# Kernel optimization log

Measured on AMD Instinct MI355X. Metric: run time of the kernel, lower is better.

## Reference

```python
import math
import jax, jax.numpy as jnp
import numpy as np

N_HEAD = 4
D_MODEL = 96
BS, N_TOK = 32, 512
A2LEN = 150          # a2len % 16 != 0 so padn > 0 (asserted in torch code)
DST_MXLEN = 32


def setup_inputs() -> dict:
    key = jax.random.key(0)
    k1, k2, k3, k4, k5, k6 = jax.random.split(key, 6)
    x = jax.random.normal(k1, (BS, N_TOK, D_MODEL), dtype=jnp.float32)
    # LinearM: w is [outdim, indim+1], last column is the bias, zeroed at init
    wqv_w = 0.02 * jax.random.normal(k2, (3 * D_MODEL, D_MODEL + 1), dtype=jnp.float32)
    wqv_w = wqv_w.at[:, -1].set(0.0)
    fanout_w = 0.02 * jax.random.normal(k3, (D_MODEL, D_MODEL + 1), dtype=jnp.float32)
    fanout_w = fanout_w.at[:, -1].set(0.0)

    def make_coo(k):
        # COO triples [dst, src, dst_cnt]; every dst has DST_MXLEN sources
        dst = jnp.repeat(jnp.arange(N_TOK), DST_MXLEN)
        src = jax.random.randint(k, (N_TOK * DST_MXLEN,), 0, N_TOK)
        cnt = jnp.tile(jnp.arange(DST_MXLEN), N_TOK)
        return jnp.stack([dst, src, cnt], axis=1).astype(jnp.int32)

    coo0 = make_coo(k4)
    coo1 = make_coo(k5)
    a2a = jnp.sort(jax.random.permutation(k6, N_TOK)[:A2LEN]).astype(jnp.int32)
    return {"x": x, "wqv_w": wqv_w, "fanout_w": fanout_w,
            "coo0": coo0, "coo1": coo1, "a2a": a2a, "dst_mxlen": DST_MXLEN}


def _linm(w, x):
    # LinearM: einsum('oi,bhi->bho') + bias column
    return jnp.einsum('oi,bti->bto', w[:, :-1], x) + w[:, -1]


def _l1attn_sparse(v, q, k, coo, dst_mxlen):
    # l1attn_sparse_cuda.L1AttnSparse: per-(dst,src) L1 scores scattered into a
    # [n_tok, dst_mxlen] ragged table (pad = -1e12), softmax over the fan-in slot.
    bs, n_tok, h, w = q.shape
    dst, src, cnt = coo[:, 0], coo[:, 1], coo[:, 2]
    scale = 1.0 / math.sqrt(w)
    ww = -jnp.sum(jnp.abs(q[:, dst] - k[:, src]), axis=-1) * scale    # [bs, cl, h]
    attn = jnp.full((bs, n_tok, dst_mxlen, h), -1e12, dtype=q.dtype)
    attn = attn.at[:, dst, cnt, :].set(ww)
    attn_sm = jax.nn.softmax(attn, axis=2)
    vw = jnp.zeros((bs, n_tok, dst_mxlen, h, w), dtype=q.dtype)
    vw = vw.at[:, dst, cnt, :, :].set(v[:, src])                      # gather by src
    return jnp.einsum('bdrh,bdrhw->bdhw', attn_sm, vw)


def _forward(x, wqv_w, fanout_w, coo0, coo1, a2a, dst_mxlen):
    bs, n_tok, width = x.shape
    h = N_HEAD
    y = _linm(wqv_w, x)
    q, k, v = jnp.split(y, 3, axis=-1)

    # --- dense all-to-all L1 attention on tokens a2a, channels 72:96 (h*6) ---
    a2len = a2a.shape[0]
    q1 = q[:, a2a, 72:].reshape(bs, a2len, h, 6)
    k1 = k[:, a2a, 72:].reshape(bs, a2len, h, 6)
    v1 = v[:, a2a, 72:].reshape(bs, a2len, h, 6)
    padl = (a2len + 15) // 16 * 16
    q2 = jnp.pad(q1, ((0, 0), (0, padl - a2len), (0, 0), (0, 0)))
    k2 = jnp.pad(k1, ((0, 0), (0, padl - a2len), (0, 0), (0, 0)))
    scale = 1.0 / math.sqrt(6)
    # l1attn_cuda.L1Attn: a[b, s, d, h] = -scale * sum_w |q[b,d,h,w] - k[b,s,h,w]|
    a = -jnp.sum(jnp.abs(q2[:, None, :, :, :] - k2[:, :, None, :, :]), axis=-1) * scale
    a = a[:, :a2len + 1, :a2len + 1, :]   # keep one zero-score pad row (attention sink)
    a = jax.nn.softmax(a, axis=1)         # softmax over src dim
    a = a[:, :a2len, :a2len, :]
    b1 = jnp.einsum('bsdh,bshw->bdhw', a, v1)
    b2 = jnp.zeros((bs, n_tok, h, 6), dtype=x.dtype).at[:, a2a].set(b1)
    dense = b2.reshape(bs, n_tok, h * 6)

    # --- two sparse COO L1-attention groups: channels 32:52 and 52:72 (h*5) ---
    sparse_out = []
    for i, coo in enumerate((coo0, coo1)):
        sta = 32 + 20 * i
        q1 = q[:, :, sta:sta + 20].reshape(bs, n_tok, h, 5)
        k1 = k[:, :, sta:sta + 20].reshape(bs, n_tok, h, 5)
        v1 = v[:, :, sta:sta + 20].reshape(bs, n_tok, h, 5)
        sparse_out.append(_l1attn_sparse(v1, q1, k1, coo, dst_mxlen).reshape(bs, n_tok, h * 5))

    # channels 0:32 are never written -> zeros
    b = jnp.concatenate([jnp.zeros((bs, n_tok, 32), dtype=x.dtype),
                         sparse_out[0], sparse_out[1], dense], axis=-1)
    yb = b * jax.nn.sigmoid(1.702 * b)    # QuickGELU
    return x + _linm(fanout_w, yb)


def reference(x, wqv_w, fanout_w, coo0, coo1, a2a, dst_mxlen):
    return _forward(x, wqv_w, fanout_w, coo0, coo1, a2a, dst_mxlen)
```

## Files before the change

kernel.cpp:

```cpp
#include <hip/hip_runtime.h>
#include <hip/hip_bf16.h>
#include <math.h>

#define BS    32
#define T     512
#define BT    (BS * T)
#define D     96
#define H     4
#define MX    32
#define A2MAX 160

#define QKV_TOK  16
#define FUSE_TOK 16
#define DT       32

__global__ void prep_kernel(const float* __restrict__ wqv, const float* __restrict__ fw,
                            const int* __restrict__ coo0, const int* __restrict__ coo1,
                            const int* __restrict__ a2a, int nedges, int a2len,
                            float* __restrict__ WT, float* __restrict__ FWT,
                            int* __restrict__ srcs, int* __restrict__ flag) {
    int idx = blockIdx.x * blockDim.x + threadIdx.x;
    if (idx < 97 * 192) {
        const int i = idx / 192, oc = idx - 192 * i;
        const int p = oc >> 6, c = oc & 63;
        WT[idx] = wqv[(p * 96 + 32 + c) * 97 + i];
        return;
    }
    idx -= 97 * 192;
    if (idx < 65 * 96) {
        const int i = idx / 96, o = idx - 96 * i;
        FWT[idx] = fw[o * 97 + 32 + i];
        return;
    }
    idx -= 65 * 96;
    if (idx < 2 * nedges) {
        const int ci = idx / nedges;
        const int e  = idx - ci * nedges;
        const int* row = (ci == 0 ? coo0 : coo1) + e * 3;
        const int dst = row[0], src = row[1], cnt = row[2];
        if (dst >= 0 && dst < T && cnt >= 0 && cnt < MX)
            srcs[(ci * T + dst) * MX + cnt] = src;
        return;
    }
    idx -= 2 * nedges;
    if (idx < a2len) flag[a2a[idx]] = idx;
}

__global__ void qkv_kernel(const float* __restrict__ x, const float* __restrict__ WT,
                           const int* __restrict__ flag,
                           float* __restrict__ Q, float* __restrict__ K,
                           float* __restrict__ V,
                           float* __restrict__ Kg, float* __restrict__ Vg) {
    const int tid  = threadIdx.x;
    const int base = blockIdx.x * QKV_TOK;
    __shared__ float xs[QKV_TOK * D];
    float4* xs4 = (float4*)xs;
    const float4* xg = (const float4*)(x + base * D);
    xs4[tid]       = xg[tid];
    xs4[tid + 192] = xg[tid + 192];
    __syncthreads();
    float acc[QKV_TOK];
    const float bias = WT[96 * 192 + tid];
    #pragma unroll
    for (int j = 0; j < QKV_TOK; ++j) acc[j] = bias;
    #pragma unroll 3
    for (int i4 = 0; i4 < 24; ++i4) {
        const float w0 = WT[(4 * i4 + 0) * 192 + tid];
        const float w1 = WT[(4 * i4 + 1) * 192 + tid];
        const float w2 = WT[(4 * i4 + 2) * 192 + tid];
        const float w3 = WT[(4 * i4 + 3) * 192 + tid];
        #pragma unroll
        for (int j = 0; j < QKV_TOK; ++j) {
            const float4 xv = xs4[j * 24 + i4];
            acc[j] += w0 * xv.x + w1 * xv.y + w2 * xv.z + w3 * xv.w;
        }
    }
    const int part = tid >> 6, c = tid & 63;
    float* out = (part == 0) ? Q : (part == 1 ? K : V);
    #pragma unroll
    for (int j = 0; j < QKV_TOK; ++j) out[(base + j) * 64 + c] = acc[j];
    if (part >= 1 && c >= 40) {
        float* g = (part == 1) ? Kg : Vg;
        const int b = base >> 9;
        #pragma unroll
        for (int j = 0; j < QKV_TOK; ++j) {
            const int ps = flag[(base + j) & (T - 1)];
            if (ps >= 0) g[(b * A2MAX + ps) * 24 + (c - 40)] = acc[j];
        }
    }
}

__global__ void sparse_kernel(const float* __restrict__ Q, const float* __restrict__ K,
                              const float* __restrict__ V, const int* __restrict__ srcs,
                              float* __restrict__ B) {
    const int b   = blockIdx.y;
    const int ci  = blockIdx.x >> 2, h = blockIdx.x & 3;
    const int base = 20 * ci + h * 5;
    const int tid  = threadIdx.x;
    __shared__ float ks[5 * T];
    __shared__ float vs[5 * T];
    for (int i = tid; i < 5 * T; i += 256) {
        const int s = i & (T - 1), w = i >> 9;
        const int g = (b * T + s) * 64 + base + w;
        ks[w * T + s] = K[g];
        vs[w * T + s] = V[g];
    }
    __syncthreads();
    const float iscale = 0.4472135954999579f;
    const int t = blockIdx.z * 256 + tid;
    const int4* sp4 = (const int4*)(srcs + (ci * T + t) * MX);
    const float* qp = Q + (b * T + t) * 64 + base;
    const float q0 = qp[0], q1 = qp[1], q2 = qp[2], q3 = qp[3], q4 = qp[4];
    float l = 0.f, o0 = 0.f, o1 = 0.f, o2 = 0.f, o3 = 0.f, o4 = 0.f;
    #pragma unroll 2
    for (int c4 = 0; c4 < MX / 4; ++c4) {
        const int4 s4 = sp4[c4];
        const int sv[4] = {s4.x, s4.y, s4.z, s4.w};
        #pragma unroll
        for (int m = 0; m < 4; ++m) {
            const int s = sv[m];
            if (s < 0) continue;
            const float sum = fabsf(q0 - ks[s]) + fabsf(q1 - ks[T + s]) +
                              fabsf(q2 - ks[2 * T + s]) + fabsf(q3 - ks[3 * T + s]) +
                              fabsf(q4 - ks[4 * T + s]);
            const float e = __expf(-sum * iscale);
            l  += e;
            o0 += e * vs[s];         o1 += e * vs[T + s];
            o2 += e * vs[2 * T + s]; o3 += e * vs[3 * T + s];
            o4 += e * vs[4 * T + s];
        }
    }
    const float inv = (l > 0.f) ? 1.f / l : 0.f;
    float* bp = B + (b * T + t) * 96 + 32 + base;
    bp[0] = o0 * inv; bp[1] = o1 * inv; bp[2] = o2 * inv;
    bp[3] = o3 * inv; bp[4] = o4 * inv;
}

__global__ void dense_kernel(const float* __restrict__ Q,
                             const float* __restrict__ Kg, const float* __restrict__ Vg,
                             const int* __restrict__ a2a,
                             int a2len, int extra, float* __restrict__ B) {
    const int b   = blockIdx.y;
    const int d0  = blockIdx.x * DT;
    const int tid = threadIdx.x;
    __shared__ int   rows[A2MAX];
    __shared__ float ks[A2MAX * 32];
    __shared__ float vs[A2MAX * 32];
    for (int i = tid; i < a2len; i += 128) rows[i] = a2a[i];
    const int nq = (a2len * 24) / 4;
    const float4* kg4 = (const float4*)(Kg + (size_t)b * A2MAX * 24);
    const float4* vg4 = (const float4*)(Vg + (size_t)b * A2MAX * 24);
    for (int idx = tid; idx < nq; idx += 128) {
        const int s = idx / 6, r = idx - 6 * s;
        const float4 kk = kg4[idx];
        const float4 vv = vg4[idx];
        const float kv[4] = {kk.x, kk.y, kk.z, kk.w};
        const float vv4[4] = {vv.x, vv.y, vv.z, vv.w};
        #pragma unroll
        for (int m = 0; m < 4; ++m) {
            const int w = r * 4 + m, hh = w / 6, ww = w - 6 * hh;
            ks[s * 32 + hh * 8 + ww] = kv[m];
            vs[s * 32 + hh * 8 + ww] = vv4[m];
        }
    }
    __syncthreads();
    const int h = tid & 3, dl = tid >> 2;
    const int d = d0 + dl;
    if (d >= a2len) return;
    const int td = rows[d];
    const float scale = 0.4082482904638631f;
    const float* qp = Q + (b * T + td) * 64 + 40 + h * 6;
    const float q0 = qp[0], q1 = qp[1], q2 = qp[2],
                q3 = qp[3], q4 = qp[4], q5 = qp[5];
    float l = 0.f, o0 = 0.f, o1 = 0.f, o2 = 0.f, o3 = 0.f, o4 = 0.f, o5 = 0.f;
    for (int s = 0; s < a2len; ++s) {
        const float4 k4 = *(const float4*)&ks[s * 32 + h * 8];
        const float2 k2 = *(const float2*)&ks[s * 32 + h * 8 + 4];
        const float sum = fabsf(q0 - k4.x) + fabsf(q1 - k4.y) + fabsf(q2 - k4.z) +
                          fabsf(q3 - k4.w) + fabsf(q4 - k2.x) + fabsf(q5 - k2.y);
        const float e = __expf(-sum * scale);
        const float4 v4 = *(const float4*)&vs[s * 32 + h * 8];
        const float2 v2 = *(const float2*)&vs[s * 32 + h * 8 + 4];
        l  += e;
        o0 += e * v4.x; o1 += e * v4.y; o2 += e * v4.z;
        o3 += e * v4.w; o4 += e * v2.x; o5 += e * v2.y;
    }
    if (extra) {
        const float sum = fabsf(q0) + fabsf(q1) + fabsf(q2) +
                          fabsf(q3) + fabsf(q4) + fabsf(q5);
        l += __expf(-sum * scale);
    }
    const float inv = 1.f / l;
    float* bp = B + (b * T + td) * 96 + 72 + h * 6;
    bp[0] = o0 * inv; bp[1] = o1 * inv; bp[2] = o2 * inv;
    bp[3] = o3 * inv; bp[4] = o4 * inv; bp[5] = o5 * inv;
}

__global__ void fuse_kernel(const float* __restrict__ x, const float* __restrict__ FWT,
                            const float* __restrict__ B, const int* __restrict__ flag,
                            float* __restrict__ out) {
    const int tid  = threadIdx.x;
    const int half = tid / 96;
    const int o    = tid - 96 * half;
    const int base = blockIdx.x * FUSE_TOK;
    __shared__ float yb[FUSE_TOK * 64];
    float4* yb4 = (float4*)yb;
    for (int idx = tid; idx < FUSE_TOK * 64; idx += 192) {
        const int j = idx >> 6, k = idx & 63;
        float v = B[(base + j) * 96 + 32 + k];
        if (k >= 40 && flag[(base + j) & (T - 1)] < 0) v = 0.f;
        yb[idx] = v / (1.f + __expf(-1.702f * v));
    }
    __syncthreads();
    float acc[FUSE_TOK / 2];
    const float bias = FWT[64 * 96 + o];
    #pragma unroll
    for (int j = 0; j < FUSE_TOK / 2; ++j) acc[j] = bias;
    #pragma unroll 2
    for (int i4 = 0; i4 < 16; ++i4) {
        const float w0 = FWT[(4 * i4 + 0) * 96 + o];
        const float w1 = FWT[(4 * i4 + 1) * 96 + o];
        const float w2 = FWT[(4 * i4 + 2) * 96 + o];
        const float w3 = FWT[(4 * i4 + 3) * 96 + o];
        #pragma unroll
        for (int j = 0; j < FUSE_TOK / 2; ++j) {
            const float4 yv = yb4[(2 * j + half) * 16 + i4];
            acc[j] += w0 * yv.x + w1 * yv.y + w2 * yv.z + w3 * yv.w;
        }
    }
    #pragma unroll
    for (int j = 0; j < FUSE_TOK / 2; ++j) {
        const int token = base + 2 * j + half;
        out[token * D + o] = x[token * D + o] + acc[j];
    }
}

extern "C" void kernel_launch(void* const* d_in, const int* in_sizes, int n_in,
                              void* d_out, int out_size, void* d_ws, size_t ws_size,
                              hipStream_t stream) {
    const float* x   = (const float*)d_in[0];
    const float* wqv = (const float*)d_in[1];
    const float* fw  = (const float*)d_in[2];
    const int*  coo0 = (const int*)d_in[3];
    const int*  coo1 = (const int*)d_in[4];
    const int*  a2a  = (const int*)d_in[5];
    int a2len        = in_sizes[5];
    if (a2len > A2MAX) a2len = A2MAX;
    const int nedges = in_sizes[3] / 3;

    float* Q   = (float*)d_ws;
    float* K   = Q  + (size_t)BT * 64;
    float* V   = K  + (size_t)BT * 64;
    float* Bb  = V  + (size_t)BT * 64;
    float* Kg  = Bb + (size_t)BT * 96;
    float* Vg  = Kg + (size_t)BS * A2MAX * 24;
    int*  srcs = (int*)(Vg + (size_t)BS * A2MAX * 24);
    int*  flag = srcs + 2 * T * MX;
    float* WT  = (float*)(flag + T);
    float* FWT = WT + 97 * 192;

    hipMemsetAsync(srcs, 0xFF, (2 * T * MX + T) * sizeof(int), stream);

    const int prep_n = 97 * 192 + 65 * 96 + 2 * nedges + a2len;
    prep_kernel<<<(prep_n + 255) / 256, 256, 0, stream>>>(
        wqv, fw, coo0, coo1, a2a, nedges, a2len, WT, FWT, srcs, flag);
    qkv_kernel<<<BT / QKV_TOK, 192, 0, stream>>>(x, WT, flag, Q, K, V, Kg, Vg);
    sparse_kernel<<<dim3(8, BS, 2), 256, 0, stream>>>(Q, K, V, srcs, Bb);
    const int padl  = (a2len + 15) / 16 * 16;
    const int extra = (padl > a2len) ? 1 : 0;
    dense_kernel<<<dim3((a2len + DT - 1) / DT, BS), 128, 0, stream>>>(
        Q, Kg, Vg, a2a, a2len, extra, Bb);
    fuse_kernel<<<BT / FUSE_TOK, 192, 0, stream>>>(x, FWT, Bb, flag, (float*)d_out);
}
```

Measured before the change: 144.1 us.

## Store sparse Q/K/V channel-major and compact dense Q to gathered rows

The QKV projection now writes the sparse-attention channels (0:40) in a channel-major [c][b][t] layout using float4 stores, and writes dense-group Q only for the a2a rows into a compact Qg buffer. The sparse kernel loads K/V into shared memory and Q into registers with coalesced row reads, and uses one 512-thread block per (batch, head, group) instead of two 256-thread blocks. This removes strided 64-float row gathers and cuts the intermediate Q/K/V footprint. In exchange there are fewer, larger sparse blocks, and each block now stages K/V once rather than twice.

```diff
diff --git a/kernel.cpp b/kernel.cpp
--- a/kernel.cpp
+++ b/kernel.cpp
@@ -48,9 +48,10 @@
 
 __global__ void qkv_kernel(const float* __restrict__ x, const float* __restrict__ WT,
                            const int* __restrict__ flag,
-                           float* __restrict__ Q, float* __restrict__ K,
-                           float* __restrict__ V,
-                           float* __restrict__ Kg, float* __restrict__ Vg) {
+                           float* __restrict__ QS, float* __restrict__ KS,
+                           float* __restrict__ VS,
+                           float* __restrict__ Qg, float* __restrict__ Kg,
+                           float* __restrict__ Vg) {
     const int tid  = threadIdx.x;
     const int base = blockIdx.x * QKV_TOK;
     __shared__ float xs[QKV_TOK * D];
@@ -76,41 +77,50 @@
         }
     }
     const int part = tid >> 6, c = tid & 63;
-    float* out = (part == 0) ? Q : (part == 1 ? K : V);
-    #pragma unroll
-    for (int j = 0; j < QKV_TOK; ++j) out[(base + j) * 64 + c] = acc[j];
-    if (part >= 1 && c >= 40) {
-        float* g = (part == 1) ? Kg : Vg;
-        const int b = base >> 9;
+    const int b    = base >> 9;
+    const int tloc = base & (T - 1);
+    if (c < 40) {
+        float* XS = (part == 0) ? QS : (part == 1 ? KS : VS);
+        float4* dp = (float4*)(XS + ((size_t)c * BS + b) * T + tloc);
+        #pragma unroll
+        for (int m = 0; m < 4; ++m)
+            dp[m] = make_float4(acc[4 * m], acc[4 * m + 1],
+                                acc[4 * m + 2], acc[4 * m + 3]);
+    } else {
+        float* g = (part == 0) ? Qg : (part == 1 ? Kg : Vg);
         #pragma unroll
         for (int j = 0; j < QKV_TOK; ++j) {
-            const int ps = flag[(base + j) & (T - 1)];
-            if (ps >= 0) g[(b * A2MAX + ps) * 24 + (c - 40)] = acc[j];
-        }
-    }
-}
-
-__global__ void sparse_kernel(const float* __restrict__ Q, const float* __restrict__ K,
-                              const float* __restrict__ V, const int* __restrict__ srcs,
+            const int ps = flag[tloc + j];
+            if (ps >= 0) g[((size_t)b * A2MAX + ps) * 24 + (c - 40)] = acc[j];
+        }
+    }
+}
+
+__global__ void sparse_kernel(const float* __restrict__ QS, const float* __restrict__ KS,
+                              const float* __restrict__ VS, const int* __restrict__ srcs,
                               float* __restrict__ B) {
     const int b   = blockIdx.y;
     const int ci  = blockIdx.x >> 2, h = blockIdx.x & 3;
-    const int base = 20 * ci + h * 5;
-    const int tid  = threadIdx.x;
+    const int cb  = 20 * ci + 5 * h;
+    const int tid = threadIdx.x;
     __shared__ float ks[5 * T];
     __shared__ float vs[5 * T];
-    for (int i = tid; i < 5 * T; i += 256) {
-        const int s = i & (T - 1), w = i >> 9;
-        const int g = (b * T + s) * 64 + base + w;
-        ks[w * T + s] = K[g];
-        vs[w * T + s] = V[g];
+    const size_t rowbase = ((size_t)cb * BS + b) * T;
+    #pragma unroll
+    for (int i = tid; i < 5 * T; i += 512) {
+        const int w = i >> 9, s = i & (T - 1);
+        ks[i] = KS[rowbase + (size_t)w * BS * T + s];
+        vs[i] = VS[rowbase + (size_t)w * BS * T + s];
     }
     __syncthreads();
     const float iscale = 0.4472135954999579f;
-    const int t = blockIdx.z * 256 + tid;
+    const int t = tid;
+    const float q0 = QS[rowbase + 0 * BS * T + t];
+    const float q1 = QS[rowbase + 1 * BS * T + t];
+    const float q2 = QS[rowbase + 2 * BS * T + t];
+    const float q3 = QS[rowbase + 3 * BS * T + t];
+    const float q4 = QS[rowbase + 4 * BS * T + t];
     const int4* sp4 = (const int4*)(srcs + (ci * T + t) * MX);
-    const float* qp = Q + (b * T + t) * 64 + base;
-    const float q0 = qp[0], q1 = qp[1], q2 = qp[2], q3 = qp[3], q4 = qp[4];
     float l = 0.f, o0 = 0.f, o1 = 0.f, o2 = 0.f, o3 = 0.f, o4 = 0.f;
     #pragma unroll 2
     for (int c4 = 0; c4 < MX / 4; ++c4) {
@@ -131,12 +141,12 @@
         }
     }
     const float inv = (l > 0.f) ? 1.f / l : 0.f;
-    float* bp = B + (b * T + t) * 96 + 32 + base;
+    float* bp = B + ((size_t)b * T + t) * 96 + 32 + cb;
     bp[0] = o0 * inv; bp[1] = o1 * inv; bp[2] = o2 * inv;
     bp[3] = o3 * inv; bp[4] = o4 * inv;
 }
 
-__global__ void dense_kernel(const float* __restrict__ Q,
+__global__ void dense_kernel(const float* __restrict__ Qg,
                              const float* __restrict__ Kg, const float* __restrict__ Vg,
                              const int* __restrict__ a2a,
                              int a2len, int extra, float* __restrict__ B) {
@@ -154,7 +164,7 @@
         const int s = idx / 6, r = idx - 6 * s;
         const float4 kk = kg4[idx];
         const float4 vv = vg4[idx];
-        const float kv[4] = {kk.x, kk.y, kk.z, kk.w};
+        const float kv[4]  = {kk.x, kk.y, kk.z, kk.w};
         const float vv4[4] = {vv.x, vv.y, vv.z, vv.w};
         #pragma unroll
         for (int m = 0; m < 4; ++m) {
@@ -167,9 +177,8 @@
     const int h = tid & 3, dl = tid >> 2;
     const int d = d0 + dl;
     if (d >= a2len) return;
-    const int td = rows[d];
     const float scale = 0.4082482904638631f;
-    const float* qp = Q + (b * T + td) * 64 + 40 + h * 6;
+    const float* qp = Qg + ((size_t)b * A2MAX + d) * 24 + h * 6;
     const float q0 = qp[0], q1 = qp[1], q2 = qp[2],
                 q3 = qp[3], q4 = qp[4], q5 = qp[5];
     float l = 0.f, o0 = 0.f, o1 = 0.f, o2 = 0.f, o3 = 0.f, o4 = 0.f, o5 = 0.f;
@@ -191,7 +200,7 @@
         l += __expf(-sum * scale);
     }
     const float inv = 1.f / l;
-    float* bp = B + (b * T + td) * 96 + 72 + h * 6;
+    float* bp = B + ((size_t)b * T + rows[d]) * 96 + 72 + h * 6;
     bp[0] = o0 * inv; bp[1] = o1 * inv; bp[2] = o2 * inv;
     bp[3] = o3 * inv; bp[4] = o4 * inv; bp[5] = o5 * inv;
 }
@@ -248,11 +257,12 @@
     if (a2len > A2MAX) a2len = A2MAX;
     const int nedges = in_sizes[3] / 3;
 
-    float* Q   = (float*)d_ws;
-    float* K   = Q  + (size_t)BT * 64;
-    float* V   = K  + (size_t)BT * 64;
-    float* Bb  = V  + (size_t)BT * 64;
-    float* Kg  = Bb + (size_t)BT * 96;
+    float* QS  = (float*)d_ws;
+    float* KS  = QS + (size_t)40 * BS * T;
+    float* VS  = KS + (size_t)40 * BS * T;
+    float* Bb  = VS + (size_t)40 * BS * T;
+    float* Qg  = Bb + (size_t)BT * 96;
+    float* Kg  = Qg + (size_t)BS * A2MAX * 24;
     float* Vg  = Kg + (size_t)BS * A2MAX * 24;
     int*  srcs = (int*)(Vg + (size_t)BS * A2MAX * 24);
     int*  flag = srcs + 2 * T * MX;
@@ -264,11 +274,11 @@
     const int prep_n = 97 * 192 + 65 * 96 + 2 * nedges + a2len;
     prep_kernel<<<(prep_n + 255) / 256, 256, 0, stream>>>(
         wqv, fw, coo0, coo1, a2a, nedges, a2len, WT, FWT, srcs, flag);
-    qkv_kernel<<<BT / QKV_TOK, 192, 0, stream>>>(x, WT, flag, Q, K, V, Kg, Vg);
-    sparse_kernel<<<dim3(8, BS, 2), 256, 0, stream>>>(Q, K, V, srcs, Bb);
+    qkv_kernel<<<BT / QKV_TOK, 192, 0, stream>>>(x, WT, flag, QS, KS, VS, Qg, Kg, Vg);
+    sparse_kernel<<<dim3(8, BS), 512, 0, stream>>>(QS, KS, VS, srcs, Bb);
     const int padl  = (a2len + 15) / 16 * 16;
     const int extra = (padl > a2len) ? 1 : 0;
     dense_kernel<<<dim3((a2len + DT - 1) / DT, BS), 128, 0, stream>>>(
-        Q, Kg, Vg, a2a, a2len, extra, Bb);
+        Qg, Kg, Vg, a2a, a2len, extra, Bb);
     fuse_kernel<<<BT / FUSE_TOK, 192, 0, stream>>>(x, FWT, Bb, flag, (float*)d_out);
 }
```

New measurement: 131.6 us. -8.7%, faster.
